# Performance work log

Hardware: AMD Instinct MI355X
Metric: run time of the kernel (lower is better)

## Reference

```python
import jax, jax.numpy as jnp
import numpy as np

H, KV, HD = 32, 4, 64
REP = H // KV
MAX_POS = 2048


def setup_inputs() -> dict:
    key = jax.random.key(0)
    ks = jax.random.split(key, 6)
    B, S, D = 2, 1024, 2048
    x = jax.random.normal(ks[0], (B, S, D), dtype=jnp.float32)
    wq = jax.random.normal(ks[1], (D, H * HD), dtype=jnp.float32) * 0.02
    wk = jax.random.normal(ks[2], (D, KV * HD), dtype=jnp.float32) * 0.02
    wv = jax.random.normal(ks[3], (D, KV * HD), dtype=jnp.float32) * 0.02
    wo = jax.random.normal(ks[4], (H * HD, D), dtype=jnp.float32) * 0.02
    # RoPE tables: [max_pos, head_dim//2]
    inv_freq = 1.0 / (10000.0 ** (np.arange(0, HD, 2, dtype=np.float32) / HD))
    angles = np.arange(MAX_POS, dtype=np.float32)[:, None] * inv_freq[None, :]
    cos = jnp.asarray(np.cos(angles), dtype=jnp.float32)
    sin = jnp.asarray(np.sin(angles), dtype=jnp.float32)
    # causal additive mask [S, S]
    row = jnp.arange(S)[:, None]
    col = jnp.arange(S)[None, :]
    mask = jnp.where(col <= row, 0.0, -1e9).astype(jnp.float32)
    return {"x": x, "wq": wq, "wk": wk, "wv": wv, "wo": wo,
            "cos": cos, "sin": sin, "mask": mask, "pos": 0}


def _rotate(t, c, s):
    # t: [B,S,Hx,HD]; c,s: [1,S,1,HD//2]
    half = t.shape[-1] // 2
    t1, t2 = t[..., :half], t[..., half:]
    return jnp.concatenate([t1 * c - t2 * s, t2 * c + t1 * s], axis=-1)


def reference(x, wq, wk, wv, wo, cos, sin, mask, pos):
    B, S, D = x.shape
    q = (x @ wq).reshape(B, S, H, HD)
    k = (x @ wk).reshape(B, S, KV, HD)
    v = (x @ wv).reshape(B, S, KV, HD)
    c = cos[pos:pos + S][None, :, None, :]
    s = sin[pos:pos + S][None, :, None, :]
    q = _rotate(q, c, s)
    k = _rotate(k, c, s)
    # prefill: cache[:, 0:S] == fresh k,v, kv_len == S
    # native GQA broadcast: group q heads by kv head instead of repeating k/v
    qg = q.reshape(B, S, KV, REP, HD)
    scores = jnp.einsum('bqkrd,bskd->bkrqs', qg, k) / jnp.sqrt(jnp.float32(HD))
    scores = scores + mask  # mask broadcasts over [B,KV,REP,S,S]
    attn = jax.nn.softmax(scores, axis=-1)
    out = jnp.einsum('bkrqs,bskd->bqkrd', attn, v).reshape(B, S, H * HD)
    return out @ wo
```

## Files before the change

### kernel.cpp

```cpp
#include <hip/hip_runtime.h>

#define B_ 2
#define S_ 1024
#define D_ 2048
#define H_ 32
#define KV_ 4
#define HD_ 64
#define NQKV 2560

typedef __attribute__((ext_vector_type(8))) short bf16x8;
typedef __attribute__((ext_vector_type(4))) float f32x4;

__device__ __forceinline__ unsigned short f2bf(float f) {
  unsigned int u = __float_as_uint(f);
  u = (u + 0x7fffu + ((u >> 16) & 1u)) >> 16;
  return (unsigned short)u;
}

__global__ __launch_bounds__(256) void k_convert(const float* __restrict__ src,
                                                 unsigned short* __restrict__ dst, int n4) {
  int i = blockIdx.x * 256 + threadIdx.x;
  if (i >= n4) return;
  float4 v = ((const float4*)src)[i];
  ushort4 o;
  o.x = f2bf(v.x); o.y = f2bf(v.y); o.z = f2bf(v.z); o.w = f2bf(v.w);
  ((ushort4*)dst)[i] = o;
}

__global__ __launch_bounds__(256) void k_transpose(const float* __restrict__ src,
                                                   unsigned short* __restrict__ dst,
                                                   int K, int N, int roff, int dld) {
  __shared__ float tile[32][33];
  int n0 = blockIdx.x * 32, k0 = blockIdx.y * 32;
  int tx = threadIdx.x & 31, ty = threadIdx.x >> 5;
  #pragma unroll
  for (int i = 0; i < 4; ++i)
    tile[ty + 8 * i][tx] = src[(size_t)(k0 + ty + 8 * i) * N + (n0 + tx)];
  __syncthreads();
  #pragma unroll
  for (int i = 0; i < 4; ++i)
    dst[(size_t)(roff + n0 + ty + 8 * i) * dld + (k0 + tx)] = f2bf(tile[tx][ty + 8 * i]);
}

template <int BM, int BN, int MODE>
__global__ __launch_bounds__(256) void k_gemm(const unsigned short* __restrict__ A,
                                              const unsigned short* __restrict__ Bt,
                                              float* __restrict__ C,
                                              const float* __restrict__ cosT,
                                              const float* __restrict__ sinT,
                                              const int* __restrict__ posp,
                                              unsigned short* __restrict__ q_r,
                                              unsigned short* __restrict__ k_r,
                                              unsigned short* __restrict__ v_t,
                                              int M, int N, int K) {
  constexpr int MR = BM / 32;
  constexpr int NR = BN / 32;
  __shared__ alignas(16) unsigned short As[BM * 64];
  __shared__ alignas(16) unsigned short Bs[BN * 64];
  const int tid = threadIdx.x;
  const int wid = tid >> 6, lane = tid & 63;
  const int lo = lane & 15, hi = lane >> 4;
  const int m0 = blockIdx.y * BM, n0 = blockIdx.x * BN;
  const int wr = wid >> 1, wc = wid & 1;
  f32x4 acc[MR][NR] = {};

  const int nkt = K >> 6;
  for (int kt = 0; kt < nkt; ++kt) {
    __syncthreads();
    #pragma unroll
    for (int u = tid; u < BM * 8; u += 256) {
      int row = u >> 3, ch = u & 7, chs = ch ^ (row & 7);
      const unsigned short* ga = A + (size_t)(m0 + row) * K + kt * 64 + chs * 8;
      __builtin_amdgcn_global_load_lds((const __attribute__((address_space(1))) void*)ga,
                                       (__attribute__((address_space(3))) void*)(As + u * 8), 16, 0, 0);
    }
    #pragma unroll
    for (int u = tid; u < BN * 8; u += 256) {
      int row = u >> 3, ch = u & 7, chs = ch ^ (row & 7);
      const unsigned short* gb = Bt + (size_t)(n0 + row) * K + kt * 64 + chs * 8;
      __builtin_amdgcn_global_load_lds((const __attribute__((address_space(1))) void*)gb,
                                       (__attribute__((address_space(3))) void*)(Bs + u * 8), 16, 0, 0);
    }
    __syncthreads();
    #pragma unroll
    for (int ks = 0; ks < 2; ++ks) {
      const int chs = (ks * 4 + hi) ^ (lo & 7);
      bf16x8 a[MR], b[NR];
      #pragma unroll
      for (int m = 0; m < MR; ++m) {
        int row = wr * (BM / 2) + m * 16 + lo;
        a[m] = *(const bf16x8*)(As + row * 64 + chs * 8);
      }
      #pragma unroll
      for (int n = 0; n < NR; ++n) {
        int row = wc * (BN / 2) + n * 16 + lo;
        b[n] = *(const bf16x8*)(Bs + row * 64 + chs * 8);
      }
      #pragma unroll
      for (int m = 0; m < MR; ++m)
        #pragma unroll
        for (int n = 0; n < NR; ++n)
          acc[m][n] = __builtin_amdgcn_mfma_f32_16x16x32_bf16(a[m], b[n], acc[m][n], 0, 0, 0);
    }
  }

  if (MODE == 0) {
    const int cr = hi * 4;
    #pragma unroll
    for (int m = 0; m < MR; ++m)
      #pragma unroll
      for (int n = 0; n < NR; ++n) {
        int col = n0 + wc * (BN / 2) + n * 16 + lo;
        int rowb = m0 + wr * (BM / 2) + m * 16 + cr;
        #pragma unroll
        for (int r = 0; r < 4; ++r)
          C[(size_t)(rowb + r) * N + col] = acc[m][n][r];
      }
  } else {
    const int col0 = n0 + wc * (BN / 2);
    const int pos = posp[0];
    if (col0 < 2048) {
      const int h = col0 >> 6;
      #pragma unroll
      for (int m = 0; m < MR; ++m)
        #pragma unroll
        for (int r = 0; r < 4; ++r) {
          int row = m0 + wr * (BM / 2) + m * 16 + hi * 4 + r;
          int s = row & (S_ - 1), b = row >> 10;
          unsigned short* base = q_r + ((size_t)(b * H_ + h) * S_ + s) * HD_;
          #pragma unroll
          for (int np = 0; np < 2; ++np) {
            int i = np * 16 + lo;
            float t1 = acc[m][np][r], t2 = acc[m][np + 2][r];
            float c = cosT[(size_t)(pos + s) * 32 + i];
            float sn = sinT[(size_t)(pos + s) * 32 + i];
            base[i] = f2bf(t1 * c - t2 * sn);
            base[i + 32] = f2bf(t2 * c + t1 * sn);
          }
        }
    } else if (col0 < 2304) {
      const int g = (col0 - 2048) >> 6;
      #pragma unroll
      for (int m = 0; m < MR; ++m)
        #pragma unroll
        for (int r = 0; r < 4; ++r) {
          int row = m0 + wr * (BM / 2) + m * 16 + hi * 4 + r;
          int s = row & (S_ - 1), b = row >> 10;
          unsigned short* base = k_r + ((size_t)(b * KV_ + g) * S_ + s) * HD_;
          #pragma unroll
          for (int np = 0; np < 2; ++np) {
            int i = np * 16 + lo;
            float t1 = acc[m][np][r], t2 = acc[m][np + 2][r];
            float c = cosT[(size_t)(pos + s) * 32 + i];
            float sn = sinT[(size_t)(pos + s) * 32 + i];
            base[i] = f2bf(t1 * c - t2 * sn);
            base[i + 32] = f2bf(t2 * c + t1 * sn);
          }
        }
    } else {
      const int g = (col0 - 2304) >> 6;
      #pragma unroll
      for (int m = 0; m < MR; ++m) {
        int row0 = m0 + wr * (BM / 2) + m * 16 + hi * 4;
        int s0 = row0 & (S_ - 1), b = row0 >> 10;
        #pragma unroll
        for (int n = 0; n < NR; ++n) {
          int d = n * 16 + lo;
          ushort4 o;
          o.x = f2bf(acc[m][n][0]);
          o.y = f2bf(acc[m][n][1]);
          o.z = f2bf(acc[m][n][2]);
          o.w = f2bf(acc[m][n][3]);
          *(ushort4*)(v_t + ((size_t)(b * KV_ + g) * HD_ + d) * S_ + s0) = o;
        }
      }
    }
  }
}

__global__ __launch_bounds__(256) void k_attn(const unsigned short* __restrict__ qr,
                                              const unsigned short* __restrict__ kr,
                                              const unsigned short* __restrict__ vt,
                                              unsigned short* __restrict__ ao) {
  __shared__ alignas(16) unsigned short k_lds[2][64 * 64];
  __shared__ alignas(16) unsigned short v_lds[2][64 * 64];
  const int tid = threadIdx.x;
  const int wid = tid >> 6, lane = tid & 63;
  const int lo = lane & 15, hi = lane >> 4;
  const int b = blockIdx.z, h = blockIdx.y, g = h >> 3;
  const float kscale = 0.125f;

  const unsigned short* kbase = kr + (size_t)(b * KV_ + g) * S_ * HD_;
  const unsigned short* vbase = vt + (size_t)(b * KV_ + g) * HD_ * S_;
  int buf = 0;

  auto stage = [&](int c, int bi) {
    const int j0 = c * 64;
    #pragma unroll
    for (int i = 0; i < 2; ++i) {
      int u = i * 256 + tid;
      int r = u >> 3, ch = u & 7;
      int chs = ch ^ (r & 7);
      const unsigned short* gk = kbase + (size_t)(j0 + r) * HD_ + chs * 8;
      __builtin_amdgcn_global_load_lds((const __attribute__((address_space(1))) void*)gk,
                                       (__attribute__((address_space(3))) void*)(k_lds[bi] + u * 8), 16, 0, 0);
      const unsigned short* gv = vbase + (size_t)r * S_ + j0 + chs * 8;
      __builtin_amdgcn_global_load_lds((const __attribute__((address_space(1))) void*)gv,
                                       (__attribute__((address_space(3))) void*)(v_lds[bi] + u * 8), 16, 0, 0);
    }
  };

  auto processTile = [&](int qt) {
    const int q = qt * 64 + wid * 16 + lo;
    const unsigned short* qrow = qr + ((size_t)(b * H_ + h) * S_ + q) * HD_;
    bf16x8 qf[2];
    qf[0] = *(const bf16x8*)(qrow + hi * 8);
    qf[1] = *(const bf16x8*)(qrow + 32 + hi * 8);

    f32x4 oacc[4] = {};
    float mrun = -1e30f, lrun = 0.f;

    stage(0, buf);
    __syncthreads();

    for (int c = 0; c <= qt; ++c) {
      if (c < qt) stage(c + 1, buf ^ 1);
      const int j0 = c * 64;
      const unsigned short* kl = k_lds[buf];
      const unsigned short* vl = v_lds[buf];

      f32x4 st[4];
      #pragma unroll
      for (int jt = 0; jt < 4; ++jt) st[jt] = (f32x4){0.f, 0.f, 0.f, 0.f};
      __builtin_amdgcn_s_setprio(1);
      #pragma unroll
      for (int ks = 0; ks < 2; ++ks)
        #pragma unroll
        for (int jt = 0; jt < 4; ++jt) {
          int row = jt * 16 + lo;
          int chs = (ks * 4 + hi) ^ (lo & 7);
          bf16x8 kf = *(const bf16x8*)(kl + row * 64 + chs * 8);
          st[jt] = __builtin_amdgcn_mfma_f32_16x16x32_bf16(kf, qf[ks], st[jt], 0, 0, 0);
        }
      __builtin_amdgcn_s_setprio(0);

      const bool diag = (c == qt);
      float pmax = -1e30f;
      #pragma unroll
      for (int jt = 0; jt < 4; ++jt)
        #pragma unroll
        for (int rr = 0; rr < 4; ++rr) {
          float sc = st[jt][rr] * kscale;
          if (diag && (j0 + jt * 16 + hi * 4 + rr > q)) sc = -1e30f;
          st[jt][rr] = sc;
          pmax = fmaxf(pmax, sc);
        }
      pmax = fmaxf(pmax, __shfl_xor(pmax, 16, 64));
      pmax = fmaxf(pmax, __shfl_xor(pmax, 32, 64));
      float mn = fmaxf(mrun, pmax);
      float scale = __expf(mrun - mn);
      float ps = 0.f;
      #pragma unroll
      for (int jt = 0; jt < 4; ++jt)
        #pragma unroll
        for (int rr = 0; rr < 4; ++rr) {
          float e = __expf(st[jt][rr] - mn);
          st[jt][rr] = e;
          ps += e;
        }
      ps += __shfl_xor(ps, 16, 64);
      ps += __shfl_xor(ps, 32, 64);
      lrun = lrun * scale + ps;
      mrun = mn;
      #pragma unroll
      for (int dt = 0; dt < 4; ++dt)
        #pragma unroll
        for (int rr = 0; rr < 4; ++rr) oacc[dt][rr] *= scale;

      unsigned int pk[4][2];
      #pragma unroll
      for (int jt = 0; jt < 4; ++jt)
        #pragma unroll
        for (int cp = 0; cp < 2; ++cp)
          pk[jt][cp] = (unsigned int)f2bf(st[jt][2 * cp]) |
                       ((unsigned int)f2bf(st[jt][2 * cp + 1]) << 16);

      int s0l = ((hi & 1) << 5) + lo;
      int s1l = s0l + 16;
      bool hb = (hi & 2) != 0;
      bf16x8 pf[2];
      #pragma unroll
      for (int ks = 0; ks < 2; ++ks) {
        unsigned int a0 = __shfl((int)pk[2 * ks][0], s0l, 64);
        unsigned int b0 = __shfl((int)pk[2 * ks + 1][0], s0l, 64);
        unsigned int a1 = __shfl((int)pk[2 * ks][1], s0l, 64);
        unsigned int b1 = __shfl((int)pk[2 * ks + 1][1], s0l, 64);
        unsigned int a2 = __shfl((int)pk[2 * ks][0], s1l, 64);
        unsigned int b2 = __shfl((int)pk[2 * ks + 1][0], s1l, 64);
        unsigned int a3 = __shfl((int)pk[2 * ks][1], s1l, 64);
        unsigned int b3 = __shfl((int)pk[2 * ks + 1][1], s1l, 64);
        union { unsigned int u[4]; bf16x8 v; } cvt;
        cvt.u[0] = hb ? b0 : a0;
        cvt.u[1] = hb ? b1 : a1;
        cvt.u[2] = hb ? b2 : a2;
        cvt.u[3] = hb ? b3 : a3;
        pf[ks] = cvt.v;
      }

      __builtin_amdgcn_s_setprio(1);
      #pragma unroll
      for (int ks = 0; ks < 2; ++ks)
        #pragma unroll
        for (int dt = 0; dt < 4; ++dt) {
          int row = dt * 16 + lo;
          int chs = (ks * 4 + hi) ^ (lo & 7);
          bf16x8 vf = *(const bf16x8*)(vl + row * 64 + chs * 8);
          oacc[dt] = __builtin_amdgcn_mfma_f32_16x16x32_bf16(vf, pf[ks], oacc[dt], 0, 0, 0);
        }
      __builtin_amdgcn_s_setprio(0);

      __syncthreads();
      if (c < qt) buf ^= 1;
    }

    float inv = 1.f / lrun;
    #pragma unroll
    for (int dt = 0; dt < 4; ++dt) {
      ushort4 o;
      o.x = f2bf(oacc[dt][0] * inv);
      o.y = f2bf(oacc[dt][1] * inv);
      o.z = f2bf(oacc[dt][2] * inv);
      o.w = f2bf(oacc[dt][3] * inv);
      *(ushort4*)(ao + ((size_t)(b * S_ + q)) * (H_ * HD_) + h * HD_ + dt * 16 + hi * 4) = o;
    }
  };

  processTile(blockIdx.x);
  processTile((S_ / 64 - 1) - blockIdx.x);
}

extern "C" void kernel_launch(void* const* d_in, const int* in_sizes, int n_in,
                              void* d_out, int out_size, void* d_ws, size_t ws_size,
                              hipStream_t stream) {
  const float* x    = (const float*)d_in[0];
  const float* wq   = (const float*)d_in[1];
  const float* wk   = (const float*)d_in[2];
  const float* wv   = (const float*)d_in[3];
  const float* wo   = (const float*)d_in[4];
  const float* cosT = (const float*)d_in[5];
  const float* sinT = (const float*)d_in[6];
  const int*   posp = (const int*)d_in[8];
  float* out = (float*)d_out;

  char* ws = (char*)d_ws;
  size_t off = 0;
  auto alloc = [&](size_t bytes) {
    char* p = ws + off;
    off += (bytes + 255) & ~(size_t)255;
    return p;
  };
  unsigned short* xb  = (unsigned short*)alloc((size_t)B_ * S_ * D_ * 2);
  unsigned short* wft = (unsigned short*)alloc((size_t)NQKV * D_ * 2);
  unsigned short* wot = (unsigned short*)alloc((size_t)D_ * D_ * 2);
  unsigned short* q_r = (unsigned short*)alloc((size_t)B_ * H_ * S_ * HD_ * 2);
  unsigned short* k_r = (unsigned short*)alloc((size_t)B_ * KV_ * S_ * HD_ * 2);
  unsigned short* v_t = (unsigned short*)alloc((size_t)B_ * KV_ * HD_ * S_ * 2);
  unsigned short* ao  = (unsigned short*)alloc((size_t)B_ * S_ * H_ * HD_ * 2);
  if (off > ws_size) return;

  k_convert<<<(B_ * S_ * D_ / 4 + 255) / 256, 256, 0, stream>>>(x, xb, B_ * S_ * D_ / 4);
  k_transpose<<<dim3(D_ / 32, D_ / 32), 256, 0, stream>>>(wq, wft, D_, D_, 0, D_);
  k_transpose<<<dim3((KV_ * HD_) / 32, D_ / 32), 256, 0, stream>>>(wk, wft, D_, KV_ * HD_, 2048, D_);
  k_transpose<<<dim3((KV_ * HD_) / 32, D_ / 32), 256, 0, stream>>>(wv, wft, D_, KV_ * HD_, 2304, D_);
  k_transpose<<<dim3(D_ / 32, D_ / 32), 256, 0, stream>>>(wo, wot, D_, D_, 0, D_);

  k_gemm<64, 128, 1><<<dim3(NQKV / 128, (B_ * S_) / 64), 256, 0, stream>>>(
      xb, wft, nullptr, cosT, sinT, posp, q_r, k_r, v_t, B_ * S_, NQKV, D_);

  k_attn<<<dim3(S_ / 128, H_, B_), 256, 0, stream>>>(q_r, k_r, v_t, ao);

  k_gemm<64, 128, 0><<<dim3(D_ / 128, (B_ * S_) / 64), 256, 0, stream>>>(
      ao, wot, out, nullptr, nullptr, nullptr, nullptr, nullptr, nullptr, B_ * S_, D_, D_);
}
```

Before: 116.7 us.

## Rewrite attention with 32x32 MFMA tiles and fuse weight transposes

The attention kernel now uses 32x32x16 MFMA, with each wave owning 32 query rows and each block owning 128 query rows. Q tiles are assigned in a balanced causal order through a flattened block id, and the causal mask is applied only on the last two KV chunks. The 1/sqrt(d) scale moves into the Q RoPE epilogue, the row-sum cross-lane reduction is deferred to the end, and the four weight-transpose launches are merged into one grid. The aim is fewer shuffles, fewer launches and more work per MFMA, at the cost of higher register pressure from the f32x16 accumulators.

Measured after the change: 114.6 us. About the same (-1.9%).

```diff
diff --git a/kernel.cpp b/kernel.cpp
--- a/kernel.cpp
+++ b/kernel.cpp
@@ -7,15 +7,21 @@
 #define KV_ 4
 #define HD_ 64
 #define NQKV 2560
+#define KVB 64
 
 typedef __attribute__((ext_vector_type(8))) short bf16x8;
 typedef __attribute__((ext_vector_type(4))) float f32x4;
+typedef __attribute__((ext_vector_type(16))) float f32x16;
 
 __device__ __forceinline__ unsigned short f2bf(float f) {
   unsigned int u = __float_as_uint(f);
   u = (u + 0x7fffu + ((u >> 16) & 1u)) >> 16;
   return (unsigned short)u;
 }
+
+#define GLOAD_LDS(gp, lp) \
+  __builtin_amdgcn_global_load_lds((const __attribute__((address_space(1))) void*)(gp), \
+                                   (__attribute__((address_space(3))) void*)(lp), 16, 0, 0)
 
 __global__ __launch_bounds__(256) void k_convert(const float* __restrict__ src,
                                                  unsigned short* __restrict__ dst, int n4) {
@@ -27,11 +33,23 @@
   ((ushort4*)dst)[i] = o;
 }
 
-__global__ __launch_bounds__(256) void k_transpose(const float* __restrict__ src,
-                                                   unsigned short* __restrict__ dst,
-                                                   int K, int N, int roff, int dld) {
+__global__ __launch_bounds__(256) void k_transpose4(const float* __restrict__ wq,
+                                                    const float* __restrict__ wk,
+                                                    const float* __restrict__ wv,
+                                                    const float* __restrict__ wo,
+                                                    unsigned short* __restrict__ wft,
+                                                    unsigned short* __restrict__ wot) {
   __shared__ float tile[32][33];
+  const int z = blockIdx.z;
+  const float* src;
+  unsigned short* dst;
+  int N, roff;
+  if (z == 0)      { src = wq; dst = wft; N = 2048; roff = 0; }
+  else if (z == 1) { src = wk; dst = wft; N = 256;  roff = 2048; }
+  else if (z == 2) { src = wv; dst = wft; N = 256;  roff = 2304; }
+  else             { src = wo; dst = wot; N = 2048; roff = 0; }
   int n0 = blockIdx.x * 32, k0 = blockIdx.y * 32;
+  if (n0 >= N) return;
   int tx = threadIdx.x & 31, ty = threadIdx.x >> 5;
   #pragma unroll
   for (int i = 0; i < 4; ++i)
@@ -39,7 +57,7 @@
   __syncthreads();
   #pragma unroll
   for (int i = 0; i < 4; ++i)
-    dst[(size_t)(roff + n0 + ty + 8 * i) * dld + (k0 + tx)] = f2bf(tile[tx][ty + 8 * i]);
+    dst[(size_t)(roff + n0 + ty + 8 * i) * D_ + (k0 + tx)] = f2bf(tile[tx][ty + 8 * i]);
 }
 
 template <int BM, int BN, int MODE>
@@ -70,16 +88,12 @@
     #pragma unroll
     for (int u = tid; u < BM * 8; u += 256) {
       int row = u >> 3, ch = u & 7, chs = ch ^ (row & 7);
-      const unsigned short* ga = A + (size_t)(m0 + row) * K + kt * 64 + chs * 8;
-      __builtin_amdgcn_global_load_lds((const __attribute__((address_space(1))) void*)ga,
-                                       (__attribute__((address_space(3))) void*)(As + u * 8), 16, 0, 0);
+      GLOAD_LDS(A + (size_t)(m0 + row) * K + kt * 64 + chs * 8, As + u * 8);
     }
     #pragma unroll
     for (int u = tid; u < BN * 8; u += 256) {
       int row = u >> 3, ch = u & 7, chs = ch ^ (row & 7);
-      const unsigned short* gb = Bt + (size_t)(n0 + row) * K + kt * 64 + chs * 8;
-      __builtin_amdgcn_global_load_lds((const __attribute__((address_space(1))) void*)gb,
-                                       (__attribute__((address_space(3))) void*)(Bs + u * 8), 16, 0, 0);
+      GLOAD_LDS(Bt + (size_t)(n0 + row) * K + kt * 64 + chs * 8, Bs + u * 8);
     }
     __syncthreads();
     #pragma unroll
@@ -134,8 +148,8 @@
             float t1 = acc[m][np][r], t2 = acc[m][np + 2][r];
             float c = cosT[(size_t)(pos + s) * 32 + i];
             float sn = sinT[(size_t)(pos + s) * 32 + i];
-            base[i] = f2bf(t1 * c - t2 * sn);
-            base[i + 32] = f2bf(t2 * c + t1 * sn);
+            base[i] = f2bf((t1 * c - t2 * sn) * 0.125f);
+            base[i + 32] = f2bf((t2 * c + t1 * sn) * 0.125f);
           }
         }
     } else if (col0 < 2304) {
@@ -182,161 +196,171 @@
                                               const unsigned short* __restrict__ kr,
                                               const unsigned short* __restrict__ vt,
                                               unsigned short* __restrict__ ao) {
-  __shared__ alignas(16) unsigned short k_lds[2][64 * 64];
-  __shared__ alignas(16) unsigned short v_lds[2][64 * 64];
+  __shared__ alignas(16) unsigned short k_lds[2][KVB * HD_];
+  __shared__ alignas(16) unsigned short v_lds[2][HD_ * KVB];
   const int tid = threadIdx.x;
   const int wid = tid >> 6, lane = tid & 63;
-  const int lo = lane & 15, hi = lane >> 4;
-  const int b = blockIdx.z, h = blockIdx.y, g = h >> 3;
-  const float kscale = 0.125f;
+  const int l31 = lane & 31, hi5 = lane >> 5;
+
+  const int fid = blockIdx.x + 8 * blockIdx.y + 256 * blockIdx.z;
+  const int half = fid >> 8, u0 = fid & 255;
+  const int i4 = u0 >> 6, hb = u0 & 63;
+  const int qt = half ? 7 - i4 : i4;
+  const int h = hb >> 1, b = hb & 1, g = h >> 3;
+
+  const int q_abs = qt * 128 + wid * 32 + l31;
+  const int nch = 2 * qt + 2;
+
+  const unsigned short* qrow = qr + ((size_t)(b * H_ + h) * S_ + q_abs) * HD_;
+  bf16x8 qf[4];
+  #pragma unroll
+  for (int ks = 0; ks < 4; ++ks)
+    qf[ks] = *(const bf16x8*)(qrow + ks * 16 + hi5 * 8);
 
   const unsigned short* kbase = kr + (size_t)(b * KV_ + g) * S_ * HD_;
   const unsigned short* vbase = vt + (size_t)(b * KV_ + g) * HD_ * S_;
+
+  f32x16 oacc[2] = {};
+  float mrun = -1e30f, ls = 0.f;
   int buf = 0;
 
   auto stage = [&](int c, int bi) {
-    const int j0 = c * 64;
-    #pragma unroll
-    for (int i = 0; i < 2; ++i) {
-      int u = i * 256 + tid;
-      int r = u >> 3, ch = u & 7;
-      int chs = ch ^ (r & 7);
-      const unsigned short* gk = kbase + (size_t)(j0 + r) * HD_ + chs * 8;
-      __builtin_amdgcn_global_load_lds((const __attribute__((address_space(1))) void*)gk,
-                                       (__attribute__((address_space(3))) void*)(k_lds[bi] + u * 8), 16, 0, 0);
-      const unsigned short* gv = vbase + (size_t)r * S_ + j0 + chs * 8;
-      __builtin_amdgcn_global_load_lds((const __attribute__((address_space(1))) void*)gv,
-                                       (__attribute__((address_space(3))) void*)(v_lds[bi] + u * 8), 16, 0, 0);
+    const int j0 = c * KVB;
+    #pragma unroll
+    for (int ii = 0; ii < 2; ++ii) {
+      int uu = ii * 256 + tid;
+      int r = uu >> 3, ch = uu & 7, chs = ch ^ (r & 7);
+      GLOAD_LDS(kbase + (size_t)(j0 + r) * HD_ + chs * 8, k_lds[bi] + uu * 8);
+    }
+    #pragma unroll
+    for (int ii = 0; ii < 2; ++ii) {
+      int uu = ii * 256 + tid;
+      int d = uu >> 3, ch = uu & 7, chs = ch ^ (d & 7);
+      GLOAD_LDS(vbase + (size_t)d * S_ + j0 + chs * 8, v_lds[bi] + uu * 8);
     }
   };
 
-  auto processTile = [&](int qt) {
-    const int q = qt * 64 + wid * 16 + lo;
-    const unsigned short* qrow = qr + ((size_t)(b * H_ + h) * S_ + q) * HD_;
-    bf16x8 qf[2];
-    qf[0] = *(const bf16x8*)(qrow + hi * 8);
-    qf[1] = *(const bf16x8*)(qrow + 32 + hi * 8);
-
-    f32x4 oacc[4] = {};
-    float mrun = -1e30f, lrun = 0.f;
-
-    stage(0, buf);
+  stage(0, 0);
+  __syncthreads();
+
+  for (int c = 0; c < nch; ++c) {
+    if (c + 1 < nch) stage(c + 1, buf ^ 1);
+    const unsigned short* kl = k_lds[buf];
+    const unsigned short* vl = v_lds[buf];
+    const int j0 = c * KVB;
+
+    f32x16 st[2] = {};
+    __builtin_amdgcn_s_setprio(1);
+    #pragma unroll
+    for (int ks = 0; ks < 4; ++ks) {
+      const int chs = ((ks * 2 + hi5) ^ (l31 & 7)) * 8;
+      #pragma unroll
+      for (int jt = 0; jt < 2; ++jt) {
+        bf16x8 kf = *(const bf16x8*)(kl + (jt * 32 + l31) * HD_ + chs);
+        st[jt] = __builtin_amdgcn_mfma_f32_32x32x16_bf16(kf, qf[ks], st[jt], 0, 0, 0);
+      }
+    }
+    __builtin_amdgcn_s_setprio(0);
+
+    float pmax = -1e30f;
+    if (c >= nch - 2) {
+      #pragma unroll
+      for (int jt = 0; jt < 2; ++jt)
+        #pragma unroll
+        for (int r = 0; r < 16; ++r) {
+          int j_abs = j0 + jt * 32 + (r & 3) + 8 * (r >> 2) + 4 * hi5;
+          if (j_abs > q_abs) st[jt][r] = -1e30f;
+          pmax = fmaxf(pmax, st[jt][r]);
+        }
+    } else {
+      #pragma unroll
+      for (int jt = 0; jt < 2; ++jt)
+        #pragma unroll
+        for (int r = 0; r < 16; ++r) pmax = fmaxf(pmax, st[jt][r]);
+    }
+    pmax = fmaxf(pmax, __shfl_xor(pmax, 32, 64));
+    float mn = fmaxf(mrun, pmax);
+    float scale = __expf(mrun - mn);
+    float lsl = 0.f;
+    #pragma unroll
+    for (int jt = 0; jt < 2; ++jt)
+      #pragma unroll
+      for (int r = 0; r < 16; ++r) {
+        float e = __expf(st[jt][r] - mn);
+        st[jt][r] = e;
+        lsl += e;
+      }
+    ls = ls * scale + lsl;
+    mrun = mn;
+    #pragma unroll
+    for (int dt = 0; dt < 2; ++dt)
+      #pragma unroll
+      for (int r = 0; r < 16; ++r) oacc[dt][r] *= scale;
+
+    unsigned int pk[2][4][2];
+    #pragma unroll
+    for (int jt = 0; jt < 2; ++jt)
+      #pragma unroll
+      for (int qd = 0; qd < 4; ++qd) {
+        pk[jt][qd][0] = (unsigned int)f2bf(st[jt][qd * 4 + 0]) |
+                        ((unsigned int)f2bf(st[jt][qd * 4 + 1]) << 16);
+        pk[jt][qd][1] = (unsigned int)f2bf(st[jt][qd * 4 + 2]) |
+                        ((unsigned int)f2bf(st[jt][qd * 4 + 3]) << 16);
+      }
+
+    bf16x8 pf[4];
+    #pragma unroll
+    for (int jt = 0; jt < 2; ++jt) {
+      unsigned int ex0a = hi5 ? pk[jt][0][0] : pk[jt][1][0];
+      unsigned int ex0b = hi5 ? pk[jt][0][1] : pk[jt][1][1];
+      unsigned int ex1a = hi5 ? pk[jt][2][0] : pk[jt][3][0];
+      unsigned int ex1b = hi5 ? pk[jt][2][1] : pk[jt][3][1];
+      unsigned int rA0 = (unsigned int)__shfl_xor((int)ex0a, 32, 64);
+      unsigned int rA1 = (unsigned int)__shfl_xor((int)ex0b, 32, 64);
+      unsigned int rB0 = (unsigned int)__shfl_xor((int)ex1a, 32, 64);
+      unsigned int rB1 = (unsigned int)__shfl_xor((int)ex1b, 32, 64);
+      union { unsigned int w[4]; bf16x8 v; } fe, fo;
+      if (hi5) {
+        fe.w[0] = rA0; fe.w[1] = rA1; fe.w[2] = pk[jt][1][0]; fe.w[3] = pk[jt][1][1];
+        fo.w[0] = rB0; fo.w[1] = rB1; fo.w[2] = pk[jt][3][0]; fo.w[3] = pk[jt][3][1];
+      } else {
+        fe.w[0] = pk[jt][0][0]; fe.w[1] = pk[jt][0][1]; fe.w[2] = rA0; fe.w[3] = rA1;
+        fo.w[0] = pk[jt][2][0]; fo.w[1] = pk[jt][2][1]; fo.w[2] = rB0; fo.w[3] = rB1;
+      }
+      pf[jt * 2 + 0] = fe.v;
+      pf[jt * 2 + 1] = fo.v;
+    }
+
+    __builtin_amdgcn_s_setprio(1);
+    #pragma unroll
+    for (int ks = 0; ks < 4; ++ks) {
+      const int chs = ((ks * 2 + hi5) ^ (l31 & 7)) * 8;
+      #pragma unroll
+      for (int dt = 0; dt < 2; ++dt) {
+        bf16x8 vf = *(const bf16x8*)(vl + (dt * 32 + l31) * KVB + chs);
+        oacc[dt] = __builtin_amdgcn_mfma_f32_32x32x16_bf16(vf, pf[ks], oacc[dt], 0, 0, 0);
+      }
+    }
+    __builtin_amdgcn_s_setprio(0);
+
     __syncthreads();
-
-    for (int c = 0; c <= qt; ++c) {
-      if (c < qt) stage(c + 1, buf ^ 1);
-      const int j0 = c * 64;
-      const unsigned short* kl = k_lds[buf];
-      const unsigned short* vl = v_lds[buf];
-
-      f32x4 st[4];
-      #pragma unroll
-      for (int jt = 0; jt < 4; ++jt) st[jt] = (f32x4){0.f, 0.f, 0.f, 0.f};
-      __builtin_amdgcn_s_setprio(1);
-      #pragma unroll
-      for (int ks = 0; ks < 2; ++ks)
-        #pragma unroll
-        for (int jt = 0; jt < 4; ++jt) {
-          int row = jt * 16 + lo;
-          int chs = (ks * 4 + hi) ^ (lo & 7);
-          bf16x8 kf = *(const bf16x8*)(kl + row * 64 + chs * 8);
-          st[jt] = __builtin_amdgcn_mfma_f32_16x16x32_bf16(kf, qf[ks], st[jt], 0, 0, 0);
-        }
-      __builtin_amdgcn_s_setprio(0);
-
-      const bool diag = (c == qt);
-      float pmax = -1e30f;
-      #pragma unroll
-      for (int jt = 0; jt < 4; ++jt)
-        #pragma unroll
-        for (int rr = 0; rr < 4; ++rr) {
-          float sc = st[jt][rr] * kscale;
-          if (diag && (j0 + jt * 16 + hi * 4 + rr > q)) sc = -1e30f;
-          st[jt][rr] = sc;
-          pmax = fmaxf(pmax, sc);
-        }
-      pmax = fmaxf(pmax, __shfl_xor(pmax, 16, 64));
-      pmax = fmaxf(pmax, __shfl_xor(pmax, 32, 64));
-      float mn = fmaxf(mrun, pmax);
-      float scale = __expf(mrun - mn);
-      float ps = 0.f;
-      #pragma unroll
-      for (int jt = 0; jt < 4; ++jt)
-        #pragma unroll
-        for (int rr = 0; rr < 4; ++rr) {
-          float e = __expf(st[jt][rr] - mn);
-          st[jt][rr] = e;
-          ps += e;
-        }
-      ps += __shfl_xor(ps, 16, 64);
-      ps += __shfl_xor(ps, 32, 64);
-      lrun = lrun * scale + ps;
-      mrun = mn;
-      #pragma unroll
-      for (int dt = 0; dt < 4; ++dt)
-        #pragma unroll
-        for (int rr = 0; rr < 4; ++rr) oacc[dt][rr] *= scale;
-
-      unsigned int pk[4][2];
-      #pragma unroll
-      for (int jt = 0; jt < 4; ++jt)
-        #pragma unroll
-        for (int cp = 0; cp < 2; ++cp)
-          pk[jt][cp] = (unsigned int)f2bf(st[jt][2 * cp]) |
-                       ((unsigned int)f2bf(st[jt][2 * cp + 1]) << 16);
-
-      int s0l = ((hi & 1) << 5) + lo;
-      int s1l = s0l + 16;
-      bool hb = (hi & 2) != 0;
-      bf16x8 pf[2];
-      #pragma unroll
-      for (int ks = 0; ks < 2; ++ks) {
-        unsigned int a0 = __shfl((int)pk[2 * ks][0], s0l, 64);
-        unsigned int b0 = __shfl((int)pk[2 * ks + 1][0], s0l, 64);
-        unsigned int a1 = __shfl((int)pk[2 * ks][1], s0l, 64);
-        unsigned int b1 = __shfl((int)pk[2 * ks + 1][1], s0l, 64);
-        unsigned int a2 = __shfl((int)pk[2 * ks][0], s1l, 64);
-        unsigned int b2 = __shfl((int)pk[2 * ks + 1][0], s1l, 64);
-        unsigned int a3 = __shfl((int)pk[2 * ks][1], s1l, 64);
-        unsigned int b3 = __shfl((int)pk[2 * ks + 1][1], s1l, 64);
-        union { unsigned int u[4]; bf16x8 v; } cvt;
-        cvt.u[0] = hb ? b0 : a0;
-        cvt.u[1] = hb ? b1 : a1;
-        cvt.u[2] = hb ? b2 : a2;
-        cvt.u[3] = hb ? b3 : a3;
-        pf[ks] = cvt.v;
-      }
-
-      __builtin_amdgcn_s_setprio(1);
-      #pragma unroll
-      for (int ks = 0; ks < 2; ++ks)
-        #pragma unroll
-        for (int dt = 0; dt < 4; ++dt) {
-          int row = dt * 16 + lo;
-          int chs = (ks * 4 + hi) ^ (lo & 7);
-          bf16x8 vf = *(const bf16x8*)(vl + row * 64 + chs * 8);
-          oacc[dt] = __builtin_amdgcn_mfma_f32_16x16x32_bf16(vf, pf[ks], oacc[dt], 0, 0, 0);
-        }
-      __builtin_amdgcn_s_setprio(0);
-
-      __syncthreads();
-      if (c < qt) buf ^= 1;
-    }
-
-    float inv = 1.f / lrun;
-    #pragma unroll
-    for (int dt = 0; dt < 4; ++dt) {
+    buf ^= 1;
+  }
+
+  float tot = ls + __shfl_xor(ls, 32, 64);
+  float inv = 1.f / tot;
+  unsigned short* orow = ao + (size_t)(b * S_ + q_abs) * (H_ * HD_) + h * HD_;
+  #pragma unroll
+  for (int dt = 0; dt < 2; ++dt)
+    #pragma unroll
+    for (int rg = 0; rg < 4; ++rg) {
       ushort4 o;
-      o.x = f2bf(oacc[dt][0] * inv);
-      o.y = f2bf(oacc[dt][1] * inv);
-      o.z = f2bf(oacc[dt][2] * inv);
-      o.w = f2bf(oacc[dt][3] * inv);
-      *(ushort4*)(ao + ((size_t)(b * S_ + q)) * (H_ * HD_) + h * HD_ + dt * 16 + hi * 4) = o;
-    }
-  };
-
-  processTile(blockIdx.x);
-  processTile((S_ / 64 - 1) - blockIdx.x);
+      o.x = f2bf(oacc[dt][rg * 4 + 0] * inv);
+      o.y = f2bf(oacc[dt][rg * 4 + 1] * inv);
+      o.z = f2bf(oacc[dt][rg * 4 + 2] * inv);
+      o.w = f2bf(oacc[dt][rg * 4 + 3] * inv);
+      *(ushort4*)(orow + dt * 32 + rg * 8 + hi5 * 4) = o;
+    }
 }
 
 extern "C" void kernel_launch(void* const* d_in, const int* in_sizes, int n_in,
@@ -369,15 +393,12 @@
   if (off > ws_size) return;
 
   k_convert<<<(B_ * S_ * D_ / 4 + 255) / 256, 256, 0, stream>>>(x, xb, B_ * S_ * D_ / 4);
-  k_transpose<<<dim3(D_ / 32, D_ / 32), 256, 0, stream>>>(wq, wft, D_, D_, 0, D_);
-  k_transpose<<<dim3((KV_ * HD_) / 32, D_ / 32), 256, 0, stream>>>(wk, wft, D_, KV_ * HD_, 2048, D_);
-  k_transpose<<<dim3((KV_ * HD_) / 32, D_ / 32), 256, 0, stream>>>(wv, wft, D_, KV_ * HD_, 2304, D_);
-  k_transpose<<<dim3(D_ / 32, D_ / 32), 256, 0, stream>>>(wo, wot, D_, D_, 0, D_);
+  k_transpose4<<<dim3(D_ / 32, D_ / 32, 4), 256, 0, stream>>>(wq, wk, wv, wo, wft, wot);
 
   k_gemm<64, 128, 1><<<dim3(NQKV / 128, (B_ * S_) / 64), 256, 0, stream>>>(
       xb, wft, nullptr, cosT, sinT, posp, q_r, k_r, v_t, B_ * S_, NQKV, D_);
 
-  k_attn<<<dim3(S_ / 128, H_, B_), 256, 0, stream>>>(q_r, k_r, v_t, ao);
+  k_attn<<<dim3(8, 32, 2), 256, 0, stream>>>(q_r, k_r, v_t, ao);
 
   k_gemm<64, 128, 0><<<dim3(D_ / 128, (B_ * S_) / 64), 256, 0, stream>>>(
       ao, wot, out, nullptr, nullptr, nullptr, nullptr, nullptr, nullptr, B_ * S_, D_, D_);
```
